# Kernel optimization log

Hardware: AMD Instinct MI355X
Metric: run time of the kernel (lower is better)

Reference implementation:

```python
import jax, jax.numpy as jnp
import numpy as np

B, K, V, D, T = 8, 4, 32000, 1024, 16
EOS, PAD = 2, 0
EOS_SCORE = 1000.0
BIG = 1e9  # suppresses beams 1..K-1 at step 0 (original starts from a single beam)


def setup_inputs() -> dict:
    key = jax.random.key(0)
    k1, k2, k3, k4 = jax.random.split(key, 4)
    s = 1.0 / np.sqrt(D)
    return {
        "words": jnp.ones((B, K), dtype=jnp.int32),  # BOS=1 on every beam
        "h0": jnp.zeros((B, K, D), dtype=jnp.float32),
        "c0": jnp.zeros((B, K, D), dtype=jnp.float32),
        "E": jax.random.normal(k1, (V, D), dtype=jnp.float32) * s,
        "Wx": jax.random.normal(k2, (D, 4 * D), dtype=jnp.float32) * s,
        "Wh": jax.random.normal(k3, (D, 4 * D), dtype=jnp.float32) * s,
        "b": jnp.zeros((4 * D,), dtype=jnp.float32),
        "Wout": jax.random.normal(k4, (D, V), dtype=jnp.float32) * s,
        "bout": jnp.zeros((V,), dtype=jnp.float32),
    }


def reference(words, h0, c0, E, Wx, Wh, b, Wout, bout):
    bidx = jnp.arange(B)[:, None]
    kidx = jnp.arange(K)[None, :]
    scores0 = jnp.concatenate(
        [jnp.zeros((B, 1), jnp.float32), jnp.full((B, K - 1), BIG, jnp.float32)], axis=1)
    buf0 = jnp.zeros((B, K, T), dtype=jnp.int32)
    stopped0 = jnp.zeros((B,), dtype=bool)

    def step(carry, j):
        w, scores, h, c, stopped, buf = carry
        # proc_word: embed -> LSTM cell -> vocab logits (vectorized over B*K beams)
        x = E[w]                                              # [B,K,D]
        gates = jnp.einsum('bkd,df->bkf', x, Wx) + jnp.einsum('bkd,df->bkf', h, Wh) + b
        i_, f_, g_, o_ = jnp.split(gates, 4, axis=-1)
        c_new = jax.nn.sigmoid(f_) * c + jax.nn.sigmoid(i_) * jnp.tanh(g_)
        h_new = jax.nn.sigmoid(o_) * jnp.tanh(c_new)
        logits = jnp.einsum('bkd,dv->bkv', h_new, Wout) + bout  # [B,K,V]
        p = -jax.nn.log_softmax(logits, axis=-1)                # negative log-probs
        neg_ps, idxs = jax.lax.top_k(-p, K)                     # K smallest per beam
        cand = (-neg_ps) + scores[:, :, None]                   # [B,K,K]
        flat = cand.reshape(B, K * K)
        wflat = idxs.reshape(B, K * K)
        neg_sel, sel = jax.lax.top_k(-flat, K)                  # K smallest over all cands
        sel_scores = -neg_sel                                   # [B,K]
        prev = sel // K                                         # originating beam
        new_w = jnp.take_along_axis(wflat, sel, axis=1)
        eos = new_w == EOS
        first_eos = eos[:, 0] & (~stopped)                      # best cand is EOS -> stop
        pen = eos & (~first_eos[:, None]) & (~stopped[:, None]) # non-best EOS penalized
        sel_scores = jnp.where(pen, EOS_SCORE, sel_scores)
        tok = jnp.where(first_eos[:, None], EOS, new_w)
        tok = jnp.where(stopped[:, None], PAD, tok)
        prevb = jnp.where(stopped[:, None], kidx, prev)         # stopped rows keep order
        buf = buf[bidx, prevb]                                  # reorder beam histories
        buf = buf.at[:, :, j].set(tok.astype(jnp.int32))
        h_new = h_new[bidx, prev]                               # gather per-beam states
        c_new = c_new[bidx, prev]
        scores = jnp.where(stopped[:, None], scores, sel_scores)
        w = jnp.where(stopped[:, None], w, new_w.astype(w.dtype))
        stopped = stopped | first_eos
        return (w, scores, h_new, c_new, stopped, buf), None

    carry0 = (words, scores0, h0, c0, stopped0, buf0)
    (_, scores, _, _, _, buf), _ = jax.lax.scan(step, carry0, jnp.arange(T))
    return buf, scores
```

## Files before the change

### kernel.cpp

```cpp
#include <hip/hip_runtime.h>
#include <math.h>
#include <float.h>

namespace {

constexpr int Bb = 8, Kk = 4, BKn = 32, Dd = 1024, Ff = 4096, Vv = 32000, Tt = 16;
constexpr int GDS = 32, GDC = 32;
constexpr int LTW = 64;
constexpr int LNB = Vv / LTW;
constexpr int LCH = 32;
constexpr int LNCH = Dd / LCH;
constexpr int NVCH = LNB;
constexpr int EOSt = 2, PADt = 0;
constexpr float BIGf = 1e9f, EOSSf = 1000.0f;

constexpr size_t OFF_HTN = 0;
constexpr size_t OFF_CB0 = OFF_HTN + (size_t)Dd * BKn;
constexpr size_t OFF_CB1 = OFF_CB0 + (size_t)BKn * Dd;
constexpr size_t OFF_GP  = OFF_CB1 + (size_t)BKn * Dd;
constexpr size_t OFF_CS  = OFF_GP  + (size_t)GDS * BKn * Ff;
constexpr size_t OFF_SC  = OFF_CS  + (size_t)NVCH * BKn * 12;
constexpr size_t OFF_INT = OFF_SC  + BKn;
constexpr int IW = 0, ISTOP = 32, IPREV = 40, IBUFA = 72, IBUFB = IBUFA + Bb * Kk * Tt;

__device__ __forceinline__ void cp16(const float* g, float* l) {
  __builtin_amdgcn_global_load_lds(
      (const __attribute__((address_space(1))) void*)g,
      (__attribute__((address_space(3))) void*)l, 16, 0, 0);
}

__device__ inline void ins4(float v, int id, float tv[4], int ti[4]) {
#pragma unroll
  for (int r = 0; r < 4; r++) {
    bool better = (v > tv[r]) || (v == tv[r] && id < ti[r]);
    if (better) { float fv = tv[r]; int fi = ti[r]; tv[r] = v; ti[r] = id; v = fv; id = fi; }
  }
}

template <int STARTOFF>
__device__ inline void merge_top4(float tv[4], int ti[4], float ov[4], int oi[4]) {
#pragma unroll
  for (int r = 0; r < 4; r++) {
    float hv = tv[0]; int hi = ti[0];
    float m = hv;
    for (int off = STARTOFF; off; off >>= 1) m = fmaxf(m, __shfl_xor(m, off));
    int c = (hv == m) ? hi : 0x7fffffff;
    for (int off = STARTOFF; off; off >>= 1) c = min(c, __shfl_xor(c, off));
    if (hv == m && hi == c) {
      tv[0] = tv[1]; ti[0] = ti[1];
      tv[1] = tv[2]; ti[1] = ti[2];
      tv[2] = tv[3]; ti[2] = ti[3];
      tv[3] = -FLT_MAX; ti[3] = 0x7fffffff;
    }
    ov[r] = m; oi[r] = c;
  }
}

__global__ __launch_bounds__(256) void initK(const int* __restrict__ words,
    const float* __restrict__ h0, const float* __restrict__ c0,
    float* __restrict__ ws) {
  int* wsi = (int*)(ws + OFF_INT);
  if (blockIdx.x < 128) {
    int g = blockIdx.x * 256 + threadIdx.x;
    int d = g >> 5, bk = g & 31;
    ws[OFF_HTN + g] = h0[(size_t)bk * Dd + d];
    ws[OFF_CB0 + g] = c0[g];
  } else {
    int t = threadIdx.x;
    if (t < BKn) {
      ws[OFF_SC + t] = ((t & 3) == 0) ? 0.f : BIGf;
      wsi[IW + t] = words[t];
      wsi[IPREV + t] = t & 3;
    }
    if (t < Bb) wsi[ISTOP + t] = 0;
    for (int i = t; i < 2 * Bb * Kk * Tt; i += 256) wsi[IBUFA + i] = 0;
  }
}

__global__ __launch_bounds__(256) void gatesK(const float* __restrict__ Wx,
    const float* __restrict__ Wh, const float* __restrict__ E,
    const float* __restrict__ hTn, const int* __restrict__ wsi,
    float* __restrict__ Gp) {
  __shared__ float xs[GDC][BKn], hs[GDC][BKn];
  int tid = threadIdx.x;
  int d0 = blockIdx.y * GDC;
  {
    int bk = tid & 31, dq = tid >> 5;
    int w = wsi[IW + bk];
    int src = (bk & ~3) | wsi[IPREV + bk];
    const float* Erow = E + (size_t)w * Dd + d0;
#pragma unroll
    for (int k = 0; k < 4; k++) {
      int d = dq * 4 + k;
      xs[d][bk] = Erow[d];
      hs[d][bk] = hTn[(size_t)(d0 + d) * BKn + src];
    }
  }
  __syncthreads();
  int ct = tid & 31, bg = tid >> 5;
  int f0 = blockIdx.x * 128 + ct * 4;
  float acc[4][4];
#pragma unroll
  for (int c = 0; c < 4; c++)
#pragma unroll
    for (int i = 0; i < 4; i++) acc[c][i] = 0.f;
#pragma unroll 4
  for (int d = 0; d < GDC; ++d) {
    float4 wx = *(const float4*)(Wx + (size_t)(d0 + d) * Ff + f0);
    float4 wh = *(const float4*)(Wh + (size_t)(d0 + d) * Ff + f0);
    float4 x4 = *(const float4*)&xs[d][bg * 4];
    float4 h4 = *(const float4*)&hs[d][bg * 4];
    float xv[4] = {x4.x, x4.y, x4.z, x4.w};
    float hv[4] = {h4.x, h4.y, h4.z, h4.w};
    float wxc[4] = {wx.x, wx.y, wx.z, wx.w};
    float whc[4] = {wh.x, wh.y, wh.z, wh.w};
#pragma unroll
    for (int c = 0; c < 4; c++)
#pragma unroll
      for (int i = 0; i < 4; i++)
        acc[c][i] = fmaf(xv[i], wxc[c], fmaf(hv[i], whc[c], acc[c][i]));
  }
#pragma unroll
  for (int i = 0; i < 4; i++) {
    int bk = bg * 4 + i;
    float4 o = {acc[0][i], acc[1][i], acc[2][i], acc[3][i]};
    *(float4*)(Gp + ((size_t)blockIdx.y * BKn + bk) * Ff + f0) = o;
  }
}

__global__ __launch_bounds__(256) void lstmK(const float* __restrict__ bvec,
    const float* __restrict__ Gp, const float* __restrict__ cPrev,
    const int* __restrict__ wsi, float* __restrict__ cNew,
    float* __restrict__ hTn) {
  __shared__ float part[4][128];
  int bk = blockIdx.x;
  int dcl = threadIdx.x & 127;
  int half = threadIdx.x >> 7;
  int dc = blockIdx.y * 128 + dcl;
  float s[4] = {0.f, 0.f, 0.f, 0.f};
#pragma unroll 4
  for (int dsl = 0; dsl < 16; dsl++) {
    int ds = half * 16 + dsl;
    const float* row = Gp + ((size_t)ds * BKn + bk) * Ff;
#pragma unroll
    for (int g = 0; g < 4; g++) s[g] += row[(size_t)g * Dd + dc];
  }
  if (half == 1) {
#pragma unroll
    for (int g = 0; g < 4; g++) part[g][dcl] = s[g];
  }
  __syncthreads();
  if (half == 0) {
    float gi = s[0] + part[0][dcl] + bvec[dc];
    float gf = s[1] + part[1][dcl] + bvec[Dd + dc];
    float gg = s[2] + part[2][dcl] + bvec[2 * Dd + dc];
    float go = s[3] + part[3][dcl] + bvec[3 * Dd + dc];
    int src = (bk & ~3) | wsi[IPREV + bk];
    float c = cPrev[(size_t)src * Dd + dc];
    float si = 1.f / (1.f + expf(-gi));
    float sf = 1.f / (1.f + expf(-gf));
    float so = 1.f / (1.f + expf(-go));
    float tg = tanhf(gg);
    float cn = sf * c + si * tg;
    float hn = so * tanhf(cn);
    cNew[(size_t)bk * Dd + dc] = cn;
    hTn[(size_t)dc * BKn + bk] = hn;
  }
}

__global__ __launch_bounds__(256) void logitsAK(const float* __restrict__ Wo,
    const float* __restrict__ bo, const float* __restrict__ hTn,
    float* __restrict__ cs) {
  __shared__ float wb[2][LCH][LTW];
  __shared__ float hb[2][LCH][BKn];
  __shared__ float sd[BKn][LTW];
  int tid = threadIdx.x;
  int lane = tid & 63, wid = tid >> 6;
  int ct = tid & 15, bg = tid >> 4;
  size_t v0 = (size_t)blockIdx.x * LTW;
  float acc[4][2];
#pragma unroll
  for (int c = 0; c < 4; c++) { acc[c][0] = 0.f; acc[c][1] = 0.f; }

  float4 b4 = *(const float4*)(bo + v0 + ct * 4);

#define STAGE(CH, B)                                                          \
  {                                                                           \
    int d0_ = (CH) * LCH;                                                     \
    _Pragma("unroll") for (int i_ = 0; i_ < 2; i_++) {                        \
      int r_ = i_ * 16 + wid * 4;                                             \
      cp16(Wo + (size_t)(d0_ + r_ + (lane >> 4)) * Vv + v0 + (lane & 15) * 4, \
           &wb[B][r_][0]);                                                    \
    }                                                                         \
    cp16(hTn + (size_t)(d0_ + wid * 8) * BKn + lane * 4, &hb[B][wid * 8][0]); \
  }

  STAGE(0, 0)
  for (int ch = 0; ch < LNCH; ch++) {
    int b = ch & 1;
    if (ch + 1 < LNCH) {
      STAGE(ch + 1, b ^ 1)
      asm volatile("s_waitcnt vmcnt(3)" ::: "memory");
    } else {
      asm volatile("s_waitcnt vmcnt(0)" ::: "memory");
    }
    __builtin_amdgcn_s_barrier();
#pragma unroll 8
    for (int d = 0; d < LCH; d++) {
      float4 w4 = *(const float4*)&wb[b][d][ct * 4];
      float2 h2 = *(const float2*)&hb[b][d][bg * 2];
      acc[0][0] = fmaf(w4.x, h2.x, acc[0][0]);
      acc[1][0] = fmaf(w4.y, h2.x, acc[1][0]);
      acc[2][0] = fmaf(w4.z, h2.x, acc[2][0]);
      acc[3][0] = fmaf(w4.w, h2.x, acc[3][0]);
      acc[0][1] = fmaf(w4.x, h2.y, acc[0][1]);
      acc[1][1] = fmaf(w4.y, h2.y, acc[1][1]);
      acc[2][1] = fmaf(w4.z, h2.y, acc[2][1]);
      acc[3][1] = fmaf(w4.w, h2.y, acc[3][1]);
    }
    __builtin_amdgcn_s_barrier();
  }
#undef STAGE

#pragma unroll
  for (int c = 0; c < 4; c++) {
    sd[bg * 2 + 0][ct * 4 + c] = acc[c][0] + ((const float*)&b4)[c];
    sd[bg * 2 + 1][ct * 4 + c] = acc[c][1] + ((const float*)&b4)[c];
  }
  __syncthreads();

  int i0 = (int)v0 + lane;
  for (int bb_ = 0; bb_ < 8; ++bb_) {
    int bk = wid * 8 + bb_;
    float v0f = sd[bk][lane];
    float m = v0f;
    for (int off = 32; off; off >>= 1) m = fmaxf(m, __shfl_xor(m, off));
    float se = expf(v0f - m);
    for (int off = 32; off; off >>= 1) se += __shfl_xor(se, off);
    float tv[4]; int ti[4];
#pragma unroll
    for (int r = 0; r < 4; r++) { tv[r] = -FLT_MAX; ti[r] = 0x7fffffff; }
    ins4(v0f, i0, tv, ti);
    float ov[4]; int oi[4];
    merge_top4<32>(tv, ti, ov, oi);
    if (lane == 0) {
      float* p = cs + ((size_t)blockIdx.x * BKn + bk) * 12;
      p[0] = m; p[1] = se;
#pragma unroll
      for (int r = 0; r < 4; r++) { p[2 + r] = ov[r]; p[6 + r] = __int_as_float(oi[r]); }
    }
  }
}

__global__ __launch_bounds__(1024) void redSelK(float* __restrict__ ws, int step) {
  __shared__ float bt_s[BKn][8];
  __shared__ int s_tok[BKn], s_prevb[BKn];
  int* wsi = (int*)(ws + OFF_INT);
  const float* cs = ws + OFF_CS;
  int tid = threadIdx.x;
  int wv = tid >> 6, lane = tid & 63;
  {
    int half = lane >> 5, l32 = lane & 31;
    int bk = wv * 2 + half;
    float tv[4]; int ti[4];
#pragma unroll
    for (int r = 0; r < 4; r++) { tv[r] = -FLT_MAX; ti[r] = 0x7fffffff; }
    float M = -FLT_MAX, ls = 0.f;
    for (int g = 0; g < 4; g++) {
      float4 pa[4], pb[4], pc[4];
      bool vv[4];
#pragma unroll
      for (int j = 0; j < 4; j++) {
        int c = l32 + 32 * (g * 4 + j);
        vv[j] = c < NVCH;
        const float* p = cs + ((size_t)c * BKn + bk) * 12;
        if (vv[j]) {
          pa[j] = *(const float4*)p;
          pb[j] = *(const float4*)(p + 4);
          pc[j] = *(const float4*)(p + 8);
        }
      }
#pragma unroll
      for (int j = 0; j < 4; j++) {
        if (vv[j]) {
          float cm = pa[j].x, csum = pa[j].y;
          if (cm > M) { ls *= expf(M - cm); M = cm; }
          ls += csum * expf(cm - M);
          ins4(pa[j].z, __float_as_int(pb[j].z), tv, ti);
          ins4(pa[j].w, __float_as_int(pb[j].w), tv, ti);
          ins4(pb[j].x, __float_as_int(pc[j].x), tv, ti);
          ins4(pb[j].y, __float_as_int(pc[j].y), tv, ti);
        }
      }
    }
    for (int off = 16; off; off >>= 1) {
      float Mo = __shfl_xor(M, off), lso = __shfl_xor(ls, off);
      float Mn = fmaxf(M, Mo);
      ls = ls * expf(M - Mn) + lso * expf(Mo - Mn);
      M = Mn;
    }
    float lse = M + logf(ls);
    float ov[4]; int oi[4];
    merge_top4<16>(tv, ti, ov, oi);
    if (l32 == 0) {
#pragma unroll
      for (int r = 0; r < 4; r++) {
        bt_s[bk][r] = lse - ov[r];
        bt_s[bk][4 + r] = __int_as_float(oi[r]);
      }
    }
  }
  __syncthreads();
  if (tid < Bb) {
    int b = tid;
    int st = wsi[ISTOP + b];
    float sc[4];
#pragma unroll
    for (int k = 0; k < 4; k++) sc[k] = ws[OFF_SC + b * 4 + k];
    float cval[16]; int ctok[16];
#pragma unroll
    for (int kb = 0; kb < 4; kb++)
#pragma unroll
      for (int r = 0; r < 4; r++) {
        cval[kb * 4 + r] = bt_s[b * 4 + kb][r] + sc[kb];
        ctok[kb * 4 + r] = __float_as_int(bt_s[b * 4 + kb][4 + r]);
      }
    float selS[4]; int selW[4], prevK[4];
    int usedMask = 0;
#pragma unroll
    for (int r = 0; r < 4; r++) {
      int best = -1; float bv = FLT_MAX;
#pragma unroll
      for (int t = 0; t < 16; t++) {
        if (!((usedMask >> t) & 1) && cval[t] < bv) { bv = cval[t]; best = t; }
      }
      usedMask |= 1 << best;
      int tok = 0;
#pragma unroll
      for (int t = 0; t < 16; t++) if (t == best) tok = ctok[t];
      selS[r] = bv; selW[r] = tok; prevK[r] = best >> 2;
    }
    bool eos[4];
#pragma unroll
    for (int r = 0; r < 4; r++) eos[r] = (selW[r] == EOSt);
    bool first = eos[0] && !st;
#pragma unroll
    for (int r = 0; r < 4; r++) if (eos[r] && !first && !st) selS[r] = EOSSf;
#pragma unroll
    for (int k = 0; k < 4; k++) {
      int tok = st ? PADt : (first ? EOSt : selW[k]);
      int pb  = st ? k : prevK[k];
      s_tok[b * 4 + k] = tok;
      s_prevb[b * 4 + k] = pb;
      if (!st) { ws[OFF_SC + b * 4 + k] = selS[k]; wsi[IW + b * 4 + k] = selW[k]; }
      wsi[IPREV + b * 4 + k] = prevK[k];
    }
    wsi[ISTOP + b] = (st || first) ? 1 : 0;
  }
  __syncthreads();
  if (tid < 512) {
    const int* br = wsi + (((step & 1) == 0) ? IBUFA : IBUFB);
    int* bw = wsi + (((step & 1) == 0) ? IBUFB : IBUFA);
    int bkk = tid >> 4, t = tid & 15;
    int pb = s_prevb[bkk];
    int src = ((bkk & ~3) | pb) * Tt + t;
    int val = br[src];
    if (t == step) val = s_tok[bkk];
    bw[tid] = val;
  }
}

__global__ __launch_bounds__(256) void outK(const float* __restrict__ ws,
                                            float* __restrict__ out) {
  const int* wsi = (const int*)(ws + OFF_INT);
  int g = blockIdx.x * 256 + threadIdx.x;
  if (g < Bb * Kk * Tt) {
    out[g] = (float)wsi[IBUFA + g];
  } else if (g < Bb * Kk * Tt + BKn) {
    out[g] = ws[OFF_SC + (g - Bb * Kk * Tt)];
  }
}

}

extern "C" void kernel_launch(void* const* d_in, const int* in_sizes, int n_in,
                              void* d_out, int out_size, void* d_ws, size_t ws_size,
                              hipStream_t stream) {
  (void)in_sizes; (void)n_in; (void)out_size; (void)ws_size;
  const int*   words = (const int*)d_in[0];
  const float* h0 = (const float*)d_in[1];
  const float* c0 = (const float*)d_in[2];
  const float* E  = (const float*)d_in[3];
  const float* Wx = (const float*)d_in[4];
  const float* Wh = (const float*)d_in[5];
  const float* bv = (const float*)d_in[6];
  const float* Wo = (const float*)d_in[7];
  const float* bo = (const float*)d_in[8];
  float* ws = (float*)d_ws;
  float* hTn = ws + OFF_HTN;
  float* cb0 = ws + OFF_CB0;
  float* cb1 = ws + OFF_CB1;
  float* Gp  = ws + OFF_GP;
  float* cs  = ws + OFF_CS;
  int*   wsi = (int*)(ws + OFF_INT);

  initK<<<129, 256, 0, stream>>>(words, h0, c0, ws);
  for (int j = 0; j < Tt; j++) {
    float* cPrev = (j & 1) ? cb1 : cb0;
    float* cNext = (j & 1) ? cb0 : cb1;
    gatesK<<<dim3(32, GDS), 256, 0, stream>>>(Wx, Wh, E, hTn, wsi, Gp);
    lstmK<<<dim3(32, 8), 256, 0, stream>>>(bv, Gp, cPrev, wsi, cNext, hTn);
    logitsAK<<<LNB, 256, 0, stream>>>(Wo, bo, hTn, cs);
    redSelK<<<1, 1024, 0, stream>>>(ws, j);
  }
  outK<<<3, 256, 0, stream>>>(ws, (float*)d_out);
}
```

Measured before the change: 1.934 ms.

## Split-K logits kernel across block halves with triple-buffered loads and 4x4 register tiles

The logits kernel now splits the D reduction between two 128-thread halves of each block, each streaming its own 512-row slice of Wout. Loads are triple-buffered with two chunks in flight, and each thread computes a 4x4 tile instead of 4x2. The two halves' partial sums are combined through shared memory with an extra barrier. This is meant to raise memory-level parallelism and FMA-per-LDS-load reuse on the bandwidth-bound Wout stream, at the cost of more LDS (about 48KB, which may lower occupancy) and an extra reduction step.

```diff
diff --git a/kernel.cpp b/kernel.cpp
--- a/kernel.cpp
+++ b/kernel.cpp
@@ -9,7 +9,7 @@
 constexpr int LTW = 64;
 constexpr int LNB = Vv / LTW;
 constexpr int LCH = 32;
-constexpr int LNCH = Dd / LCH;
+constexpr int LNCHH = 16;
 constexpr int NVCH = LNB;
 constexpr int EOSt = 2, PADt = 0;
 constexpr float BIGf = 1e9f, EOSSf = 1000.0f;
@@ -171,64 +171,97 @@
 __global__ __launch_bounds__(256) void logitsAK(const float* __restrict__ Wo,
     const float* __restrict__ bo, const float* __restrict__ hTn,
     float* __restrict__ cs) {
-  __shared__ float wb[2][LCH][LTW];
-  __shared__ float hb[2][LCH][BKn];
+  __shared__ float wb[2][3][LCH][LTW];
+  __shared__ float hb[2][3][LCH][BKn];
   __shared__ float sd[BKn][LTW];
   int tid = threadIdx.x;
-  int lane = tid & 63, wid = tid >> 6;
-  int ct = tid & 15, bg = tid >> 4;
+  int half = tid >> 7;
+  int htid = tid & 127;
+  int hw = htid >> 6;
+  int lane = tid & 63;
+  int cg = htid & 15;
+  int bg = htid >> 4;
   size_t v0 = (size_t)blockIdx.x * LTW;
-  float acc[4][2];
-#pragma unroll
-  for (int c = 0; c < 4; c++) { acc[c][0] = 0.f; acc[c][1] = 0.f; }
-
-  float4 b4 = *(const float4*)(bo + v0 + ct * 4);
-
-#define STAGE(CH, B)                                                          \
-  {                                                                           \
-    int d0_ = (CH) * LCH;                                                     \
-    _Pragma("unroll") for (int i_ = 0; i_ < 2; i_++) {                        \
-      int r_ = i_ * 16 + wid * 4;                                             \
-      cp16(Wo + (size_t)(d0_ + r_ + (lane >> 4)) * Vv + v0 + (lane & 15) * 4, \
-           &wb[B][r_][0]);                                                    \
-    }                                                                         \
-    cp16(hTn + (size_t)(d0_ + wid * 8) * BKn + lane * 4, &hb[B][wid * 8][0]); \
+  int dh0 = half * 512;
+  float acc[4][4];
+#pragma unroll
+  for (int c = 0; c < 4; c++)
+#pragma unroll
+    for (int i = 0; i < 4; i++) acc[c][i] = 0.f;
+
+  float4 b4 = *(const float4*)(bo + v0 + cg * 4);
+
+#define STAGE(CH, B)                                                           \
+  {                                                                            \
+    int d0_ = dh0 + (CH) * LCH;                                                \
+    _Pragma("unroll") for (int i_ = 0; i_ < 4; i_++) {                         \
+      int db_ = hw * 16 + i_ * 4;                                              \
+      cp16(Wo + (size_t)(d0_ + db_ + (lane >> 4)) * Vv + v0 + (lane & 15) * 4, \
+           &wb[half][B][db_][0]);                                              \
+    }                                                                          \
+    _Pragma("unroll") for (int j_ = 0; j_ < 2; j_++) {                         \
+      int db_ = hw * 16 + j_ * 8;                                              \
+      cp16(hTn + (size_t)(d0_ + db_ + (lane >> 3)) * BKn + (lane & 7) * 4,     \
+           &hb[half][B][db_][0]);                                              \
+    }                                                                          \
   }
 
   STAGE(0, 0)
-  for (int ch = 0; ch < LNCH; ch++) {
-    int b = ch & 1;
-    if (ch + 1 < LNCH) {
-      STAGE(ch + 1, b ^ 1)
-      asm volatile("s_waitcnt vmcnt(3)" ::: "memory");
+  STAGE(1, 1)
+  for (int k = 0; k < LNCHH; k++) {
+    int b = k % 3;
+    if (k + 2 < LNCHH) {
+      STAGE(k + 2, (k + 2) % 3)
+      asm volatile("s_waitcnt vmcnt(12)" ::: "memory");
+    } else if (k + 1 < LNCHH) {
+      asm volatile("s_waitcnt vmcnt(6)" ::: "memory");
     } else {
       asm volatile("s_waitcnt vmcnt(0)" ::: "memory");
     }
     __builtin_amdgcn_s_barrier();
 #pragma unroll 8
     for (int d = 0; d < LCH; d++) {
-      float4 w4 = *(const float4*)&wb[b][d][ct * 4];
-      float2 h2 = *(const float2*)&hb[b][d][bg * 2];
-      acc[0][0] = fmaf(w4.x, h2.x, acc[0][0]);
-      acc[1][0] = fmaf(w4.y, h2.x, acc[1][0]);
-      acc[2][0] = fmaf(w4.z, h2.x, acc[2][0]);
-      acc[3][0] = fmaf(w4.w, h2.x, acc[3][0]);
-      acc[0][1] = fmaf(w4.x, h2.y, acc[0][1]);
-      acc[1][1] = fmaf(w4.y, h2.y, acc[1][1]);
-      acc[2][1] = fmaf(w4.z, h2.y, acc[2][1]);
-      acc[3][1] = fmaf(w4.w, h2.y, acc[3][1]);
+      float4 w4 = *(const float4*)&wb[half][b][d][cg * 4];
+      float4 h4 = *(const float4*)&hb[half][b][d][bg * 4];
+      acc[0][0] = fmaf(w4.x, h4.x, acc[0][0]);
+      acc[1][0] = fmaf(w4.y, h4.x, acc[1][0]);
+      acc[2][0] = fmaf(w4.z, h4.x, acc[2][0]);
+      acc[3][0] = fmaf(w4.w, h4.x, acc[3][0]);
+      acc[0][1] = fmaf(w4.x, h4.y, acc[0][1]);
+      acc[1][1] = fmaf(w4.y, h4.y, acc[1][1]);
+      acc[2][1] = fmaf(w4.z, h4.y, acc[2][1]);
+      acc[3][1] = fmaf(w4.w, h4.y, acc[3][1]);
+      acc[0][2] = fmaf(w4.x, h4.z, acc[0][2]);
+      acc[1][2] = fmaf(w4.y, h4.z, acc[1][2]);
+      acc[2][2] = fmaf(w4.z, h4.z, acc[2][2]);
+      acc[3][2] = fmaf(w4.w, h4.z, acc[3][2]);
+      acc[0][3] = fmaf(w4.x, h4.w, acc[0][3]);
+      acc[1][3] = fmaf(w4.y, h4.w, acc[1][3]);
+      acc[2][3] = fmaf(w4.z, h4.w, acc[2][3]);
+      acc[3][3] = fmaf(w4.w, h4.w, acc[3][3]);
     }
     __builtin_amdgcn_s_barrier();
   }
 #undef STAGE
 
-#pragma unroll
-  for (int c = 0; c < 4; c++) {
-    sd[bg * 2 + 0][ct * 4 + c] = acc[c][0] + ((const float*)&b4)[c];
-    sd[bg * 2 + 1][ct * 4 + c] = acc[c][1] + ((const float*)&b4)[c];
-  }
-  __syncthreads();
-
+  if (half == 0) {
+#pragma unroll
+    for (int c = 0; c < 4; c++)
+#pragma unroll
+      for (int i = 0; i < 4; i++)
+        sd[bg * 4 + i][cg * 4 + c] = acc[c][i] + ((const float*)&b4)[c];
+  }
+  __syncthreads();
+  if (half == 1) {
+#pragma unroll
+    for (int c = 0; c < 4; c++)
+#pragma unroll
+      for (int i = 0; i < 4; i++)
+        sd[bg * 4 + i][cg * 4 + c] += acc[c][i];
+  }
+  __syncthreads();
+
+  int wid = tid >> 6;
   int i0 = (int)v0 + lane;
   for (int bb_ = 0; bb_ < 8; ++bb_) {
     int bk = wid * 8 + bb_;
```

Measured after the change: 1.780 ms. 1.09x faster.

## Use single-wave logits blocks with 8x4 register tiles and triple-buffered LDS

Applied to the files above, without the earlier changes.

The vocab-logits kernel changes from 256-thread blocks to a single 64-thread wavefront per 64-column tile. Each thread now accumulates an 8x4 output tile instead of 4x2, which raises FMA work per LDS read. LDS staging becomes a three-deep async-copy pipeline with no workgroup barriers, since one wave owns the whole block. In exchange the block has a quarter of the threads and more registers per thread, so latency hiding depends on fitting more blocks per CU. The epilogue's per-beam reductions now run serially in one wave.

```diff
diff --git a/kernel.cpp b/kernel.cpp
--- a/kernel.cpp
+++ b/kernel.cpp
@@ -9,7 +9,7 @@
 constexpr int LTW = 64;
 constexpr int LNB = Vv / LTW;
 constexpr int LCH = 32;
-constexpr int LNCH = Dd / LCH;
+constexpr int LNCH = 32;
 constexpr int NVCH = LNB;
 constexpr int EOSt = 2, PADt = 0;
 constexpr float BIGf = 1e9f, EOSSf = 1000.0f;
@@ -168,71 +168,74 @@
   }
 }
 
-__global__ __launch_bounds__(256) void logitsAK(const float* __restrict__ Wo,
+__global__ __launch_bounds__(64) void logitsAK(const float* __restrict__ Wo,
     const float* __restrict__ bo, const float* __restrict__ hTn,
     float* __restrict__ cs) {
-  __shared__ float wb[2][LCH][LTW];
-  __shared__ float hb[2][LCH][BKn];
+  __shared__ float wb[3][LCH][LTW];
+  __shared__ float hb[3][LCH][BKn];
   __shared__ float sd[BKn][LTW];
-  int tid = threadIdx.x;
-  int lane = tid & 63, wid = tid >> 6;
-  int ct = tid & 15, bg = tid >> 4;
+  int t = threadIdx.x;
+  int cg = t & 7;
+  int bg = t >> 3;
   size_t v0 = (size_t)blockIdx.x * LTW;
-  float acc[4][2];
-#pragma unroll
-  for (int c = 0; c < 4; c++) { acc[c][0] = 0.f; acc[c][1] = 0.f; }
-
-  float4 b4 = *(const float4*)(bo + v0 + ct * 4);
+  float acc[8][4];
+#pragma unroll
+  for (int c = 0; c < 8; c++)
+#pragma unroll
+    for (int i = 0; i < 4; i++) acc[c][i] = 0.f;
+
+  float4 b4a = *(const float4*)(bo + v0 + cg * 8);
+  float4 b4b = *(const float4*)(bo + v0 + cg * 8 + 4);
 
 #define STAGE(CH, B)                                                          \
   {                                                                           \
     int d0_ = (CH) * LCH;                                                     \
-    _Pragma("unroll") for (int i_ = 0; i_ < 2; i_++) {                        \
-      int r_ = i_ * 16 + wid * 4;                                             \
-      cp16(Wo + (size_t)(d0_ + r_ + (lane >> 4)) * Vv + v0 + (lane & 15) * 4, \
-           &wb[B][r_][0]);                                                    \
-    }                                                                         \
-    cp16(hTn + (size_t)(d0_ + wid * 8) * BKn + lane * 4, &hb[B][wid * 8][0]); \
+    _Pragma("unroll") for (int k_ = 0; k_ < 8; k_++)                          \
+      cp16(Wo + (size_t)(d0_ + k_ * 4 + (t >> 4)) * Vv + v0 + (t & 15) * 4,   \
+           &wb[B][k_ * 4][0]);                                                \
+    _Pragma("unroll") for (int k_ = 0; k_ < 4; k_++)                          \
+      cp16(hTn + (size_t)(d0_ + k_ * 8 + (t >> 3)) * BKn + (t & 7) * 4,       \
+           &hb[B][k_ * 8][0]);                                                \
   }
 
   STAGE(0, 0)
-  for (int ch = 0; ch < LNCH; ch++) {
-    int b = ch & 1;
-    if (ch + 1 < LNCH) {
-      STAGE(ch + 1, b ^ 1)
-      asm volatile("s_waitcnt vmcnt(3)" ::: "memory");
+  STAGE(1, 1)
+  for (int k = 0; k < LNCH; k++) {
+    int b = k % 3;
+    if (k + 2 < LNCH) {
+      STAGE(k + 2, (k + 2) % 3)
+      asm volatile("s_waitcnt vmcnt(24)" ::: "memory");
+    } else if (k + 1 < LNCH) {
+      asm volatile("s_waitcnt vmcnt(12)" ::: "memory");
     } else {
       asm volatile("s_waitcnt vmcnt(0)" ::: "memory");
     }
-    __builtin_amdgcn_s_barrier();
 #pragma unroll 8
     for (int d = 0; d < LCH; d++) {
-      float4 w4 = *(const float4*)&wb[b][d][ct * 4];
-      float2 h2 = *(const float2*)&hb[b][d][bg * 2];
-      acc[0][0] = fmaf(w4.x, h2.x, acc[0][0]);
-      acc[1][0] = fmaf(w4.y, h2.x, acc[1][0]);
-      acc[2][0] = fmaf(w4.z, h2.x, acc[2][0]);
-      acc[3][0] = fmaf(w4.w, h2.x, acc[3][0]);
-      acc[0][1] = fmaf(w4.x, h2.y, acc[0][1]);
-      acc[1][1] = fmaf(w4.y, h2.y, acc[1][1]);
-      acc[2][1] = fmaf(w4.z, h2.y, acc[2][1]);
-      acc[3][1] = fmaf(w4.w, h2.y, acc[3][1]);
-    }
-    __builtin_amdgcn_s_barrier();
+      float4 wlo = *(const float4*)&wb[b][d][cg * 8];
+      float4 whi = *(const float4*)&wb[b][d][cg * 8 + 4];
+      float4 h4  = *(const float4*)&hb[b][d][bg * 4];
+      float wv[8] = {wlo.x, wlo.y, wlo.z, wlo.w, whi.x, whi.y, whi.z, whi.w};
+      float hv[4] = {h4.x, h4.y, h4.z, h4.w};
+#pragma unroll
+      for (int c = 0; c < 8; c++)
+#pragma unroll
+        for (int i = 0; i < 4; i++)
+          acc[c][i] = fmaf(wv[c], hv[i], acc[c][i]);
+    }
   }
 #undef STAGE
 
-#pragma unroll
-  for (int c = 0; c < 4; c++) {
-    sd[bg * 2 + 0][ct * 4 + c] = acc[c][0] + ((const float*)&b4)[c];
-    sd[bg * 2 + 1][ct * 4 + c] = acc[c][1] + ((const float*)&b4)[c];
-  }
-  __syncthreads();
-
-  int i0 = (int)v0 + lane;
-  for (int bb_ = 0; bb_ < 8; ++bb_) {
-    int bk = wid * 8 + bb_;
-    float v0f = sd[bk][lane];
+  float bb[8] = {b4a.x, b4a.y, b4a.z, b4a.w, b4b.x, b4b.y, b4b.z, b4b.w};
+#pragma unroll
+  for (int c = 0; c < 8; c++)
+#pragma unroll
+    for (int i = 0; i < 4; i++)
+      sd[bg * 4 + i][cg * 8 + c] = acc[c][i] + bb[c];
+
+  int i0 = (int)v0 + t;
+  for (int bk = 0; bk < BKn; ++bk) {
+    float v0f = sd[bk][t];
     float m = v0f;
     for (int off = 32; off; off >>= 1) m = fmaxf(m, __shfl_xor(m, off));
     float se = expf(v0f - m);
@@ -243,7 +246,7 @@
     ins4(v0f, i0, tv, ti);
     float ov[4]; int oi[4];
     merge_top4<32>(tv, ti, ov, oi);
-    if (lane == 0) {
+    if (t == 0) {
       float* p = cs + ((size_t)blockIdx.x * BKn + bk) * 12;
       p[0] = m; p[1] = se;
 #pragma unroll
@@ -410,7 +413,7 @@
     float* cNext = (j & 1) ? cb0 : cb1;
     gatesK<<<dim3(32, GDS), 256, 0, stream>>>(Wx, Wh, E, hTn, wsi, Gp);
     lstmK<<<dim3(32, 8), 256, 0, stream>>>(bv, Gp, cPrev, wsi, cNext, hTn);
-    logitsAK<<<LNB, 256, 0, stream>>>(Wo, bo, hTn, cs);
+    logitsAK<<<LNB, 64, 0, stream>>>(Wo, bo, hTn, cs);
     redSelK<<<1, 1024, 0, stream>>>(ws, j);
   }
   outK<<<3, 256, 0, stream>>>(ws, (float*)d_out);
```

After: 3.040 ms. +57.2%, slower.

## Split logits reduction dimension across waves with per-wave triple-buffered LDS pipelines

Applied to the files above, without the earlier changes.

The logits kernel now gives each of the four waves its own quarter of the hidden dimension, and each thread computes a 4x8 output tile instead of 4x2. Each wave runs an independent triple-buffered async-copy pipeline with no block-wide barriers inside the loop. The partial sums are then reduced through shared memory in four serialized steps. This raises FMA work per LDS load and removes barrier stalls. In exchange it uses more registers and LDS, which may lower occupancy, and adds a serialized cross-wave reduction.

```diff
diff --git a/kernel.cpp b/kernel.cpp
--- a/kernel.cpp
+++ b/kernel.cpp
@@ -8,8 +8,8 @@
 constexpr int GDS = 32, GDC = 32;
 constexpr int LTW = 64;
 constexpr int LNB = Vv / LTW;
-constexpr int LCH = 32;
-constexpr int LNCH = Dd / LCH;
+constexpr int LQC = 16;
+constexpr int LQN = 16;
 constexpr int NVCH = LNB;
 constexpr int EOSt = 2, PADt = 0;
 constexpr float BIGf = 1e9f, EOSSf = 1000.0f;
@@ -171,67 +171,89 @@
 __global__ __launch_bounds__(256) void logitsAK(const float* __restrict__ Wo,
     const float* __restrict__ bo, const float* __restrict__ hTn,
     float* __restrict__ cs) {
-  __shared__ float wb[2][LCH][LTW];
-  __shared__ float hb[2][LCH][BKn];
+  __shared__ float wb[4][3][LQC][LTW];
+  __shared__ float hb[4][3][LQC][BKn];
   __shared__ float sd[BKn][LTW];
   int tid = threadIdx.x;
-  int lane = tid & 63, wid = tid >> 6;
-  int ct = tid & 15, bg = tid >> 4;
+  int q = tid >> 6;
+  int lane = tid & 63;
+  int cg = lane & 15;
+  int bg = lane >> 4;
   size_t v0 = (size_t)blockIdx.x * LTW;
-  float acc[4][2];
-#pragma unroll
-  for (int c = 0; c < 4; c++) { acc[c][0] = 0.f; acc[c][1] = 0.f; }
-
-  float4 b4 = *(const float4*)(bo + v0 + ct * 4);
+  int dq0 = q * 256;
+  float acc[4][8];
+#pragma unroll
+  for (int c = 0; c < 4; c++)
+#pragma unroll
+    for (int i = 0; i < 8; i++) acc[c][i] = 0.f;
+
+  float4 b4 = *(const float4*)(bo + v0 + cg * 4);
 
 #define STAGE(CH, B)                                                          \
   {                                                                           \
-    int d0_ = (CH) * LCH;                                                     \
-    _Pragma("unroll") for (int i_ = 0; i_ < 2; i_++) {                        \
-      int r_ = i_ * 16 + wid * 4;                                             \
-      cp16(Wo + (size_t)(d0_ + r_ + (lane >> 4)) * Vv + v0 + (lane & 15) * 4, \
-           &wb[B][r_][0]);                                                    \
-    }                                                                         \
-    cp16(hTn + (size_t)(d0_ + wid * 8) * BKn + lane * 4, &hb[B][wid * 8][0]); \
+    int d0_ = dq0 + (CH) * LQC;                                               \
+    _Pragma("unroll") for (int i_ = 0; i_ < 4; i_++)                          \
+      cp16(Wo + (size_t)(d0_ + i_ * 4 + (lane >> 4)) * Vv + v0 +              \
+               (lane & 15) * 4,                                               \
+           &wb[q][B][i_ * 4][0]);                                             \
+    _Pragma("unroll") for (int j_ = 0; j_ < 2; j_++)                          \
+      cp16(hTn + (size_t)(d0_ + j_ * 8 + (lane >> 3)) * BKn + (lane & 7) * 4, \
+           &hb[q][B][j_ * 8][0]);                                             \
   }
 
   STAGE(0, 0)
-  for (int ch = 0; ch < LNCH; ch++) {
-    int b = ch & 1;
-    if (ch + 1 < LNCH) {
-      STAGE(ch + 1, b ^ 1)
-      asm volatile("s_waitcnt vmcnt(3)" ::: "memory");
+  STAGE(1, 1)
+  for (int k = 0; k < LQN; k++) {
+    int b = k % 3;
+    if (k + 2 < LQN) {
+      STAGE(k + 2, (k + 2) % 3)
+      asm volatile("s_waitcnt vmcnt(12)" ::: "memory");
+    } else if (k + 1 < LQN) {
+      asm volatile("s_waitcnt vmcnt(6)" ::: "memory");
     } else {
       asm volatile("s_waitcnt vmcnt(0)" ::: "memory");
     }
-    __builtin_amdgcn_s_barrier();
-#pragma unroll 8
-    for (int d = 0; d < LCH; d++) {
-      float4 w4 = *(const float4*)&wb[b][d][ct * 4];
-      float2 h2 = *(const float2*)&hb[b][d][bg * 2];
-      acc[0][0] = fmaf(w4.x, h2.x, acc[0][0]);
-      acc[1][0] = fmaf(w4.y, h2.x, acc[1][0]);
-      acc[2][0] = fmaf(w4.z, h2.x, acc[2][0]);
-      acc[3][0] = fmaf(w4.w, h2.x, acc[3][0]);
-      acc[0][1] = fmaf(w4.x, h2.y, acc[0][1]);
-      acc[1][1] = fmaf(w4.y, h2.y, acc[1][1]);
-      acc[2][1] = fmaf(w4.z, h2.y, acc[2][1]);
-      acc[3][1] = fmaf(w4.w, h2.y, acc[3][1]);
-    }
-    __builtin_amdgcn_s_barrier();
+    __builtin_amdgcn_sched_barrier(0);
+#pragma unroll 4
+    for (int d = 0; d < LQC; d++) {
+      float4 w4  = *(const float4*)&wb[q][b][d][cg * 4];
+      float4 hlo = *(const float4*)&hb[q][b][d][bg * 8];
+      float4 hhi = *(const float4*)&hb[q][b][d][bg * 8 + 4];
+      float wv[4] = {w4.x, w4.y, w4.z, w4.w};
+      float hv[8] = {hlo.x, hlo.y, hlo.z, hlo.w, hhi.x, hhi.y, hhi.z, hhi.w};
+#pragma unroll
+      for (int c = 0; c < 4; c++)
+#pragma unroll
+        for (int i = 0; i < 8; i++)
+          acc[c][i] = fmaf(wv[c], hv[i], acc[c][i]);
+    }
   }
 #undef STAGE
 
-#pragma unroll
-  for (int c = 0; c < 4; c++) {
-    sd[bg * 2 + 0][ct * 4 + c] = acc[c][0] + ((const float*)&b4)[c];
-    sd[bg * 2 + 1][ct * 4 + c] = acc[c][1] + ((const float*)&b4)[c];
+  float bb[4] = {b4.x, b4.y, b4.z, b4.w};
+  if (q == 0) {
+#pragma unroll
+    for (int c = 0; c < 4; c++)
+#pragma unroll
+      for (int i = 0; i < 8; i++)
+        sd[bg * 8 + i][cg * 4 + c] = acc[c][i] + bb[c];
   }
   __syncthreads();
+#pragma unroll
+  for (int qq = 1; qq < 4; qq++) {
+    if (q == qq) {
+#pragma unroll
+      for (int c = 0; c < 4; c++)
+#pragma unroll
+        for (int i = 0; i < 8; i++)
+          sd[bg * 8 + i][cg * 4 + c] += acc[c][i];
+    }
+    __syncthreads();
+  }
 
   int i0 = (int)v0 + lane;
   for (int bb_ = 0; bb_ < 8; ++bb_) {
-    int bk = wid * 8 + bb_;
+    int bk = q * 8 + bb_;
     float v0f = sd[bk][lane];
     float m = v0f;
     for (int off = 32; off; off >>= 1) m = fmaxf(m, __shfl_xor(m, off));
```

Result: faster. 1.729 ms (-10.6%).
